# Kernel tuning notes

Measured on AMD Instinct MI355X. Metric: run time of the kernel, lower is better.

Reference implementation:

```python
import jax, jax.numpy as jnp
import numpy as np

N = 8192
IN_F = 512
OUT_F = 64
NEG_SLOPE = 0.01  # nn.LeakyReLU default
MASK_VAL = -1e9


def setup_inputs() -> dict:
    key = jax.random.key(0)
    k_h, k_adj, k_W, k_a = jax.random.split(key, 4)
    h = jax.random.normal(k_h, (N, IN_F), dtype=jnp.float32)
    adjacency = jax.random.randint(k_adj, (N, N), 0, 2, dtype=jnp.int32)
    # xavier_uniform bounds
    bW = float(np.sqrt(6.0 / (IN_F + OUT_F)))
    ba = float(np.sqrt(6.0 / (2 * OUT_F + 1)))
    W = jax.random.uniform(k_W, (IN_F, OUT_F), minval=-bW, maxval=bW, dtype=jnp.float32)
    a = jax.random.uniform(k_a, (2 * OUT_F, 1), minval=-ba, maxval=ba, dtype=jnp.float32)
    return {"h": h, "adjacency": adjacency, "W": W, "a": a}


def reference(h, adjacency, W, a):
    WH = h @ W                                  # [N, out_f]
    wh1 = WH @ a[:OUT_F, :]                     # [N, 1]
    wh2 = WH @ a[OUT_F:, :]                     # [N, 1]
    e = jax.nn.leaky_relu(wh1 + wh2.T, negative_slope=NEG_SLOPE)  # [N, N]
    attnt = jnp.where(adjacency > 0, e, jnp.float32(MASK_VAL))
    attnt = jax.nn.softmax(attnt, axis=1)       # row-wise softmax
    hfirst = attnt @ WH                         # [N, out_f]
    return jax.nn.elu(hfirst)
```

## Files before the change

kernel.cpp:

```cpp
#include <hip/hip_runtime.h>
#include <hip/hip_bf16.h>

#define N 8192
#define IN_F 512
#define OUT_F 64
#define S_SPLIT 4
#define JT (N / S_SPLIT)
#define SUBC 512
#define NSUB (JT / SUBC)
#define LDP 536
#define LOG2E 1.44269504088896340736f

typedef __attribute__((ext_vector_type(8))) short short8;
typedef __attribute__((ext_vector_type(4))) float floatx4;
typedef __attribute__((ext_vector_type(4))) int intx4;

__device__ inline short f2bf(float x) {
    __hip_bfloat16 b = __float2bfloat16(x);
    return __builtin_bit_cast(short, b);
}

__device__ inline float fexp2(float x) {
#if __has_builtin(__builtin_amdgcn_exp2f)
    return __builtin_amdgcn_exp2f(x);
#else
    return exp2f(x);
#endif
}

__global__ void k_wt(const float* __restrict__ W, short* __restrict__ WT) {
    int idx = blockIdx.x * 256 + threadIdx.x;
    int k = idx >> 6, f = idx & 63;
    WT[f * IN_F + k] = f2bf(W[k * OUT_F + f]);
}

__global__ __launch_bounds__(64) void k_wh(const float* __restrict__ h,
                                           const short* __restrict__ WT,
                                           const float* __restrict__ a,
                                           short* __restrict__ WHbT,
                                           float* __restrict__ wh1,
                                           float* __restrict__ wh2) {
    __shared__ float tile[OUT_F][17];
    int lane = threadIdx.x;
    int n = lane & 15, q = lane >> 4;
    int i0 = blockIdx.x * 16;
    int rowA = i0 + n;
    const float* hp = h + (size_t)rowA * IN_F + q * 8;
    floatx4 acc[4] = {};
#pragma unroll
    for (int k0 = 0; k0 < IN_F; k0 += 32) {
        floatx4 h0 = *(const floatx4*)(hp + k0);
        floatx4 h1 = *(const floatx4*)(hp + k0 + 4);
        short8 af;
#pragma unroll
        for (int j = 0; j < 4; j++) { af[j] = f2bf(h0[j]); af[j + 4] = f2bf(h1[j]); }
#pragma unroll
        for (int b = 0; b < 4; b++) {
            short8 bf_ = *(const short8*)(WT + (b * 16 + n) * IN_F + k0 + q * 8);
            acc[b] = __builtin_amdgcn_mfma_f32_16x16x32_bf16(af, bf_, acc[b], 0, 0, 0);
        }
    }
#pragma unroll
    for (int b = 0; b < 4; b++)
#pragma unroll
        for (int r = 0; r < 4; r++)
            tile[b * 16 + n][q * 4 + r] = acc[b][r];
    float a1v[4], a2v[4];
#pragma unroll
    for (int b = 0; b < 4; b++) { a1v[b] = a[b * 16 + n]; a2v[b] = a[OUT_F + b * 16 + n]; }
#pragma unroll
    for (int r = 0; r < 4; r++) {
        float s1 = 0.f, s2 = 0.f;
#pragma unroll
        for (int b = 0; b < 4; b++) { s1 += acc[b][r] * a1v[b]; s2 += acc[b][r] * a2v[b]; }
#pragma unroll
        for (int m = 1; m <= 8; m <<= 1) {
            s1 += __shfl_xor(s1, m, 64);
            s2 += __shfl_xor(s2, m, 64);
        }
        if (n == 0) {
            wh1[i0 + q * 4 + r] = s1 * LOG2E;
            wh2[i0 + q * 4 + r] = s2 * LOG2E;
        }
    }
    __syncthreads();
    const float* tc = tile[lane];
    short8 s0, s1v;
#pragma unroll
    for (int k = 0; k < 8; k++) { s0[k] = f2bf(tc[k]); s1v[k] = f2bf(tc[k + 8]); }
    *(short8*)(WHbT + (size_t)lane * N + i0) = s0;
    *(short8*)(WHbT + (size_t)lane * N + i0 + 8) = s1v;
}

__global__ __launch_bounds__(256, 2) void k_attn(const int* __restrict__ adj,
                                                 const short* __restrict__ WHbT,
                                                 const float* __restrict__ wh1,
                                                 const float* __restrict__ wh2,
                                                 float* __restrict__ num_part,
                                                 float* __restrict__ den_part) {
    __shared__ short ldsb[OUT_F * LDP];
    int tid = threadIdx.x;
    int w = tid >> 6;
    int lane = tid & 63;
    int n = lane & 15, q = lane >> 4;
    int split = blockIdx.y;
    int j0 = split * JT;
    int i0 = blockIdx.x * 64 + w * 16;

    float wh1f = wh1[i0 + n];

    floatx4 acc[4] = {};
    floatx4 accd = {};
    const short* lp = ldsb + q * 8;

    short8 onesf = {};
    if (n == 0) {
        short o = f2bf(1.0f);
#pragma unroll
        for (int jj = 0; jj < 8; jj++) onesf[jj] = o;
    }

    const int* rowp = adj + (size_t)(i0 + n) * N + j0 + q * 8;

    intx4 A0, A1, B0, B1;

    auto loads = [&](intx4& D0, intx4& D1, int sub, int s) {
        const int* pp = rowp + sub * SUBC + s * 32;
        D0 = *(const intx4*)pp;
        D1 = *(const intx4*)(pp + 4);
    };

    auto step = [&](const intx4& D0, const intx4& D1, const float* w2p, int s) {
        floatx4 w20 = *(const floatx4*)(w2p + s * 32);
        floatx4 w21 = *(const floatx4*)(w2p + s * 32 + 4);
        short8 bfr[4];
#pragma unroll
        for (int b = 0; b < 4; b++)
            bfr[b] = *(const short8*)(lp + (b * 16 + n) * LDP + s * 32);
        float p[8];
#pragma unroll
        for (int jj = 0; jj < 8; jj++) {
            float e = wh1f + ((jj < 4) ? w20[jj] : w21[jj - 4]);
            float el = fmaxf(e, 0.01f * e);
            int av = (jj < 4) ? D0[jj] : D1[jj - 4];
            el = (av > 0) ? el : -1024.0f;
            p[jj] = fexp2(el);
        }
        short8 af;
#pragma unroll
        for (int jj = 0; jj < 8; jj++) af[jj] = f2bf(p[jj]);
#pragma unroll
        for (int b = 0; b < 4; b++)
            acc[b] = __builtin_amdgcn_mfma_f32_16x16x32_bf16(af, bfr[b], acc[b], 0, 0, 0);
        accd = __builtin_amdgcn_mfma_f32_16x16x32_bf16(af, onesf, accd, 0, 0, 0);
    };

    loads(A0, A1, 0, 0);
    for (int sub = 0; sub < NSUB; sub++) {
        __syncthreads();
#pragma unroll
        for (int l = 0; l < 16; l++) {
            int idx = l * 256 + tid;
            int f = idx >> 6, c16 = idx & 63;
            short8 v = *(const short8*)(WHbT + (size_t)f * N + j0 + sub * SUBC + c16 * 8);
            *(short8*)(ldsb + f * LDP + c16 * 8) = v;
        }
        __syncthreads();

        const float* w2p = wh2 + j0 + sub * SUBC + q * 8;
#pragma unroll
        for (int sp = 0; sp < 8; sp++) {
            int s0 = sp * 2;
            loads(B0, B1, sub, s0 + 1);
            step(A0, A1, w2p, s0);
            if (sp < 7) {
                loads(A0, A1, sub, s0 + 2);
            } else {
                loads(A0, A1, (sub + 1) & (NSUB - 1), 0);
            }
            step(B0, B1, w2p, s0 + 1);
        }
    }

    if (n == 0)
        *(floatx4*)(den_part + (size_t)split * N + i0 + q * 4) = accd;

    float* np_ = num_part + (size_t)split * N * OUT_F;
#pragma unroll
    for (int b = 0; b < 4; b++)
#pragma unroll
        for (int r = 0; r < 4; r++)
            np_[(size_t)(i0 + q * 4 + r) * OUT_F + b * 16 + n] = acc[b][r];
}

__global__ void k_final(const float* __restrict__ num_part,
                        const float* __restrict__ den_part,
                        float* __restrict__ out) {
    int idx = blockIdx.x * 256 + threadIdx.x;
    int row = idx >> 6;
    float s = 0.f, d = 0.f;
#pragma unroll
    for (int sp = 0; sp < S_SPLIT; sp++) {
        s += num_part[(size_t)sp * N * OUT_F + idx];
        d += den_part[sp * N + row];
    }
    float x = s / d;
    out[idx] = (x > 0.f) ? x : (__expf(x) - 1.f);
}

extern "C" void kernel_launch(void* const* d_in, const int* in_sizes, int n_in,
                              void* d_out, int out_size, void* d_ws, size_t ws_size,
                              hipStream_t stream) {
    const float* h = (const float*)d_in[0];
    const int* adj = (const int*)d_in[1];
    const float* W = (const float*)d_in[2];
    const float* a = (const float*)d_in[3];
    float* out = (float*)d_out;

    char* ws = (char*)d_ws;
    short* WHbT     = (short*)(ws);
    short* WT       = (short*)(ws + (size_t)(1 << 20));
    float* wh1      = (float*)(ws + (size_t)(1 << 20) + (64 << 10));
    float* wh2      = wh1 + N;
    float* num_p    = (float*)(ws + (size_t)(16 << 20));
    float* den_p    = (float*)(ws + (size_t)(48 << 20));

    k_wt<<<dim3(128), dim3(256), 0, stream>>>(W, WT);
    k_wh<<<dim3(N / 16), dim3(64), 0, stream>>>(h, WT, a, WHbT, wh1, wh2);
    k_attn<<<dim3(N / 64, S_SPLIT), dim3(256), 0, stream>>>(adj, WHbT, wh1, wh2,
                                                            num_p, den_p);
    k_final<<<dim3((N * OUT_F) / 256), dim3(256), 0, stream>>>(num_p, den_p, out);
}
```

Baseline: 441.3 us.

## Drop LDS staging of WH in attention kernel and prefetch directly from global

The attention kernel no longer stages WH tiles into shared memory with block-wide barriers. Each wave now loads its B fragments straight from global memory, and a deeper software pipeline keeps adjacency loads two steps ahead. The column split doubles to 8 and launch bounds ask for 4 blocks per CU, raising occupancy and parallelism. The cost is redundant WH reads across waves, which now rely on L2/L1 caching, plus more partial sums written and reduced in the final kernel.

```diff
diff --git a/kernel.cpp b/kernel.cpp
--- a/kernel.cpp
+++ b/kernel.cpp
@@ -4,11 +4,8 @@
 #define N 8192
 #define IN_F 512
 #define OUT_F 64
-#define S_SPLIT 4
+#define S_SPLIT 8
 #define JT (N / S_SPLIT)
-#define SUBC 512
-#define NSUB (JT / SUBC)
-#define LDP 536
 #define LOG2E 1.44269504088896340736f
 
 typedef __attribute__((ext_vector_type(8))) short short8;
@@ -92,13 +89,12 @@
     *(short8*)(WHbT + (size_t)lane * N + i0 + 8) = s1v;
 }
 
-__global__ __launch_bounds__(256, 2) void k_attn(const int* __restrict__ adj,
+__global__ __launch_bounds__(256, 4) void k_attn(const int* __restrict__ adj,
                                                  const short* __restrict__ WHbT,
                                                  const float* __restrict__ wh1,
                                                  const float* __restrict__ wh2,
                                                  float* __restrict__ num_part,
                                                  float* __restrict__ den_part) {
-    __shared__ short ldsb[OUT_F * LDP];
     int tid = threadIdx.x;
     int w = tid >> 6;
     int lane = tid & 63;
@@ -111,7 +107,6 @@
 
     floatx4 acc[4] = {};
     floatx4 accd = {};
-    const short* lp = ldsb + q * 8;
 
     short8 onesf = {};
     if (n == 0) {
@@ -121,22 +116,24 @@
     }
 
     const int* rowp = adj + (size_t)(i0 + n) * N + j0 + q * 8;
-
-    intx4 A0, A1, B0, B1;
-
-    auto loads = [&](intx4& D0, intx4& D1, int sub, int s) {
-        const int* pp = rowp + sub * SUBC + s * 32;
+    const short* bbase = WHbT + j0 + q * 8;
+    const float* w2p = wh2 + j0 + q * 8;
+
+    auto aload = [&](intx4& D0, intx4& D1, int s) {
+        const int* pp = rowp + (s & 31) * 32;
         D0 = *(const intx4*)pp;
         D1 = *(const intx4*)(pp + 4);
     };
-
-    auto step = [&](const intx4& D0, const intx4& D1, const float* w2p, int s) {
-        floatx4 w20 = *(const floatx4*)(w2p + s * 32);
-        floatx4 w21 = *(const floatx4*)(w2p + s * 32 + 4);
-        short8 bfr[4];
+    auto bload = [&](short8* bb, int s) {
+        const short* bp = bbase + (s & 31) * 32;
 #pragma unroll
         for (int b = 0; b < 4; b++)
-            bfr[b] = *(const short8*)(lp + (b * 16 + n) * LDP + s * 32);
+            bb[b] = *(const short8*)(bp + (size_t)(b * 16 + n) * N);
+    };
+    auto step = [&](const intx4& D0, const intx4& D1, const short8* bb, int s) {
+        int sc = (s & 31) * 32;
+        floatx4 w20 = *(const floatx4*)(w2p + sc);
+        floatx4 w21 = *(const floatx4*)(w2p + sc + 4);
         float p[8];
 #pragma unroll
         for (int jj = 0; jj < 8; jj++) {
@@ -151,35 +148,21 @@
         for (int jj = 0; jj < 8; jj++) af[jj] = f2bf(p[jj]);
 #pragma unroll
         for (int b = 0; b < 4; b++)
-            acc[b] = __builtin_amdgcn_mfma_f32_16x16x32_bf16(af, bfr[b], acc[b], 0, 0, 0);
+            acc[b] = __builtin_amdgcn_mfma_f32_16x16x32_bf16(af, bb[b], acc[b], 0, 0, 0);
         accd = __builtin_amdgcn_mfma_f32_16x16x32_bf16(af, onesf, accd, 0, 0, 0);
     };
 
-    loads(A0, A1, 0, 0);
-    for (int sub = 0; sub < NSUB; sub++) {
-        __syncthreads();
-#pragma unroll
-        for (int l = 0; l < 16; l++) {
-            int idx = l * 256 + tid;
-            int f = idx >> 6, c16 = idx & 63;
-            short8 v = *(const short8*)(WHbT + (size_t)f * N + j0 + sub * SUBC + c16 * 8);
-            *(short8*)(ldsb + f * LDP + c16 * 8) = v;
-        }
-        __syncthreads();
-
-        const float* w2p = wh2 + j0 + sub * SUBC + q * 8;
-#pragma unroll
-        for (int sp = 0; sp < 8; sp++) {
-            int s0 = sp * 2;
-            loads(B0, B1, sub, s0 + 1);
-            step(A0, A1, w2p, s0);
-            if (sp < 7) {
-                loads(A0, A1, sub, s0 + 2);
-            } else {
-                loads(A0, A1, (sub + 1) & (NSUB - 1), 0);
-            }
-            step(B0, B1, w2p, s0 + 1);
-        }
+    intx4 A0d0, A0d1, A1d0, A1d1, A2d0, A2d1, A3d0, A3d1;
+    short8 b0[4], b1[4];
+    aload(A0d0, A0d1, 0);
+    aload(A1d0, A1d1, 1);
+    bload(b0, 0);
+    for (int g = 0; g < 8; g++) {
+        int s0 = g * 4;
+        bload(b1, s0 + 1); aload(A2d0, A2d1, s0 + 2); step(A0d0, A0d1, b0, s0);
+        bload(b0, s0 + 2); aload(A3d0, A3d1, s0 + 3); step(A1d0, A1d1, b1, s0 + 1);
+        bload(b1, s0 + 3); aload(A0d0, A0d1, s0 + 4); step(A2d0, A2d1, b0, s0 + 2);
+        bload(b0, s0 + 4); aload(A1d0, A1d1, s0 + 5); step(A3d0, A3d1, b1, s0 + 3);
     }
 
     if (n == 0)
```

Result: no change. 438.0 us (-0.8%).
